# Optimization experiments

Hardware: AMD Instinct MI355X
Metric: run time of the kernel (lower is better)

The kernel has to match this reference:

```python
import jax, jax.numpy as jnp
import numpy as np

B, L, D = 8, 2048, 64


def setup_inputs() -> dict:
    key = jax.random.key(0)
    kq, kk, kv = jax.random.split(key, 3)
    query = jax.random.normal(kq, (B, L, D), dtype=jnp.float32)
    key_t = jax.random.normal(kk, (B, L, D), dtype=jnp.float32)
    value = jax.random.normal(kv, (B, L, D), dtype=jnp.float32)
    return {"query": query, "key": key_t, "value": value}


def reference(query, key, value):
    d = query.shape[-1]
    # e = Q K^T / sqrt(d_k)   -> [B, Lq, Lk]
    scale = 1.0 / np.sqrt(float(d)).astype(np.float32)
    e = jnp.einsum("bqd,bkd->bqk", query, key) * scale
    # stable softmax over keys (matches exp(e - max)/sum in source)
    attention = jax.nn.softmax(e, axis=-1)
    # v = A V   -> [B, Lq, Dv]
    return jnp.einsum("bqk,bkd->bqd", attention, value)
```

## Files before the change

kernel.cpp:

```cpp
#include <hip/hip_runtime.h>


#define B_ 8
#define L_ 2048
#define D_ 64
#define NT 256
#define TK 32

typedef _Float16 half8_t __attribute__((ext_vector_type(8)));
typedef _Float16 half2v __attribute__((ext_vector_type(2)));
typedef int int4v __attribute__((ext_vector_type(4)));
typedef float f32x4 __attribute__((ext_vector_type(4)));

#define SCALE_LOG2E 0.1803368801111244f

__global__ __launch_bounds__(NT) void prepass(
    const float* __restrict__ K, const float* __restrict__ V,
    _Float16* __restrict__ K16, _Float16* __restrict__ VT16)
{
    const int blk = blockIdx.x;
    const int t = threadIdx.x;
    if (blk < 512) {
        const int i = blk * NT + t;
        const float4* s4 = (const float4*)K;
        const float4 a = s4[2 * i], b = s4[2 * i + 1];
        half8_t w;
        w[0] = (_Float16)a.x; w[1] = (_Float16)a.y;
        w[2] = (_Float16)a.z; w[3] = (_Float16)a.w;
        w[4] = (_Float16)b.x; w[5] = (_Float16)b.y;
        w[6] = (_Float16)b.z; w[7] = (_Float16)b.w;
        ((half8_t*)K16)[i] = w;
    } else {
        __shared__ __align__(16) _Float16 Lt[64 * 72];
        const int vblk = blk - 512;
        const int bb = vblk >> 5;
        const int kt = vblk & 31;
        const int r  = t >> 2;
        const int ch = t & 3;
        const float* vrow = V + ((size_t)bb * L_ + kt * 64 + r) * D_ + ch * 16;
        #pragma unroll
        for (int i = 0; i < 4; ++i) {
            const float4 f = ((const float4*)vrow)[i];
            const int d0 = ch * 16 + i * 4;
            Lt[(d0 + 0) * 72 + r] = (_Float16)f.x;
            Lt[(d0 + 1) * 72 + r] = (_Float16)f.y;
            Lt[(d0 + 2) * 72 + r] = (_Float16)f.z;
            Lt[(d0 + 3) * 72 + r] = (_Float16)f.w;
        }
        __syncthreads();
        const int d  = t >> 2;
        const int c2 = t & 3;
        const half8_t w0 = *(const half8_t*)&Lt[d * 72 + c2 * 16];
        const half8_t w1 = *(const half8_t*)&Lt[d * 72 + c2 * 16 + 8];
        _Float16* orow = VT16 + ((size_t)bb * D_ + d) * L_ + kt * 64 + c2 * 16;
        *(half8_t*)orow = w0;
        *(half8_t*)(orow + 8) = w1;
    }
}


#define LOADT(KB, BK, BV)                                                       \
    {                                                                           \
        _Pragma("unroll") for (int s = 0; s < 2; ++s)                           \
        _Pragma("unroll") for (int c = 0; c < 2; ++c)                           \
            BK[s][c] = *(const half8_t*)&Kb[(size_t)((KB) + s * 16 + l15) * D_ + c * 32 + quad * 8]; \
        _Pragma("unroll") for (int d = 0; d < 4; ++d)                           \
            BV[d] = *(const half8_t*)&Vb[(size_t)(d * 16 + l15) * L_ + (KB) + quad * 8]; \
    }

#define PROC(BK, BV)                                                            \
    {                                                                           \
        f32x4 sc[2][2];                                                         \
        _Pragma("unroll") for (int ks = 0; ks < 2; ++ks)                        \
        _Pragma("unroll") for (int qs = 0; qs < 2; ++qs) {                      \
            f32x4 acc = (f32x4){0.f, 0.f, 0.f, 0.f};                            \
            acc = __builtin_amdgcn_mfma_f32_16x16x32_f16(BK[ks][0], bq[qs][0], acc, 0, 0, 0); \
            acc = __builtin_amdgcn_mfma_f32_16x16x32_f16(BK[ks][1], bq[qs][1], acc, 0, 0, 0); \
            sc[ks][qs] = acc;                                                   \
        }                                                                       \
        int pk[2][2][2];                                                        \
        _Pragma("unroll") for (int ks = 0; ks < 2; ++ks)                        \
        _Pragma("unroll") for (int qs = 0; qs < 2; ++qs) {                      \
            const float p0 = __builtin_exp2f(sc[ks][qs][0]);                    \
            const float p1 = __builtin_exp2f(sc[ks][qs][1]);                    \
            const float p2 = __builtin_exp2f(sc[ks][qs][2]);                    \
            const float p3 = __builtin_exp2f(sc[ks][qs][3]);                    \
            lacc[qs] += (p0 + p1) + (p2 + p3);                                  \
            half2v h01; h01[0] = (_Float16)p0; h01[1] = (_Float16)p1;           \
            half2v h23; h23[0] = (_Float16)p2; h23[1] = (_Float16)p3;           \
            pk[ks][qs][0] = __builtin_bit_cast(int, h01);                       \
            pk[ks][qs][1] = __builtin_bit_cast(int, h23);                       \
        }                                                                       \
        _Pragma("unroll") for (int qs = 0; qs < 2; ++qs) {                      \
            const int srcA = ((quad & 1) << 5) + l15;                           \
            const int srcB = srcA + 16;                                         \
            const int a0 = __shfl(pk[0][qs][0], srcA, 64);                      \
            const int b0 = __shfl(pk[1][qs][0], srcA, 64);                      \
            const int a1 = __shfl(pk[0][qs][1], srcA, 64);                      \
            const int b1 = __shfl(pk[1][qs][1], srcA, 64);                      \
            const int a2 = __shfl(pk[0][qs][0], srcB, 64);                      \
            const int b2 = __shfl(pk[1][qs][0], srcB, 64);                      \
            const int a3 = __shfl(pk[0][qs][1], srcB, 64);                      \
            const int b3 = __shfl(pk[1][qs][1], srcB, 64);                      \
            const bool hi = quad >= 2;                                          \
            int4v dw;                                                           \
            dw[0] = hi ? b0 : a0; dw[1] = hi ? b1 : a1;                         \
            dw[2] = hi ? b2 : a2; dw[3] = hi ? b3 : a3;                         \
            const half8_t ap = __builtin_bit_cast(half8_t, dw);                 \
            _Pragma("unroll") for (int d = 0; d < 4; ++d)                       \
                ofr[qs][d] = __builtin_amdgcn_mfma_f32_16x16x32_f16(ap, BV[d], ofr[qs][d], 0, 0, 0); \
        }                                                                       \
    }

__global__ __launch_bounds__(NT) void attn_bp(
    const float* __restrict__ Q,
    const _Float16* __restrict__ K16,
    const _Float16* __restrict__ VT16,
    float* __restrict__ O)
{
    __shared__ float Ored[256 * 33];
    __shared__ float Lred[128];

    const int t    = threadIdx.x;
    const int wave = t >> 6;
    const int lane = t & 63;
    const int quad = lane >> 4;
    const int l15  = lane & 15;

    const int b   = blockIdx.x & 7;
    const int qbi = blockIdx.x >> 3;
    const int qb  = qbi * 32;
    const int key0 = wave * (TK * 16);

    const _Float16* Kb = K16 + (size_t)b * L_ * D_;
    const _Float16* Vb = VT16 + (size_t)b * D_ * L_;

    half8_t bq[2][2];
    #pragma unroll
    for (int qs = 0; qs < 2; ++qs) {
        const float* qp = Q + ((size_t)b * L_ + qb + qs * 16 + l15) * D_ + quad * 8;
        #pragma unroll
        for (int c = 0; c < 2; ++c) {
            const float4 f0 = *(const float4*)(qp + c * 32);
            const float4 f1 = *(const float4*)(qp + c * 32 + 4);
            bq[qs][c][0] = (_Float16)(f0.x * SCALE_LOG2E);
            bq[qs][c][1] = (_Float16)(f0.y * SCALE_LOG2E);
            bq[qs][c][2] = (_Float16)(f0.z * SCALE_LOG2E);
            bq[qs][c][3] = (_Float16)(f0.w * SCALE_LOG2E);
            bq[qs][c][4] = (_Float16)(f1.x * SCALE_LOG2E);
            bq[qs][c][5] = (_Float16)(f1.y * SCALE_LOG2E);
            bq[qs][c][6] = (_Float16)(f1.z * SCALE_LOG2E);
            bq[qs][c][7] = (_Float16)(f1.w * SCALE_LOG2E);
        }
    }

    f32x4 ofr[2][4];
    #pragma unroll
    for (int qs = 0; qs < 2; ++qs)
        #pragma unroll
        for (int d = 0; d < 4; ++d)
            ofr[qs][d] = (f32x4){0.f, 0.f, 0.f, 0.f};
    float lacc[2] = {0.f, 0.f};

    half8_t bkA[2][2], bvA[4], bkB[2][2], bvB[4];
    LOADT(key0, bkA, bvA);
    for (int it = 0; it < 8; ++it) {
        const int kb = key0 + it * 64;
        LOADT(kb + 32, bkB, bvB);
        PROC(bkA, bvA);
        LOADT(kb + 64, bkA, bvA);
        PROC(bkB, bvB);
    }

    #pragma unroll
    for (int qs = 0; qs < 2; ++qs) {
        float v = lacc[qs];
        v += __shfl_xor(v, 16, 64);
        v += __shfl_xor(v, 32, 64);
        lacc[qs] = v;
    }
    if (quad == 0) {
        Lred[wave * 32 + l15] = lacc[0];
        Lred[wave * 32 + 16 + l15] = lacc[1];
    }

    #pragma unroll
    for (int qs = 0; qs < 2; ++qs)
        #pragma unroll
        for (int d = 0; d < 4; ++d)
            #pragma unroll
            for (int r = 0; r < 4; ++r)
                Ored[(wave * 64 + lane) * 33 + qs * 16 + d * 4 + r] = ofr[qs][d][r];
    __syncthreads();

    #pragma unroll
    for (int qs = 0; qs < 2; ++qs)
        #pragma unroll
        for (int r = 0; r < 4; ++r) {
            float osum = 0.f;
            #pragma unroll
            for (int w2 = 0; w2 < 4; ++w2)
                osum += Ored[(w2 * 64 + lane) * 33 + qs * 16 + wave * 4 + r];
            const int row = qs * 16 + quad * 4 + r;
            const float lt = Lred[row] + Lred[32 + row] + Lred[64 + row] + Lred[96 + row];
            O[((size_t)b * L_ + qb + row) * D_ + wave * 16 + l15] = osum / lt;
        }
}

#define KS 72
__global__ __launch_bounds__(NT) void attn_mfma_f16(
    const float* __restrict__ Q, const float* __restrict__ K,
    const float* __restrict__ V, float* __restrict__ O)
{
    __shared__ __align__(16) _Float16 Kt[64 * KS];
    __shared__ __align__(16) _Float16 Vt[D_ * KS];
    __shared__ __align__(16) _Float16 Pt[4][16 * KS];

    const int t = threadIdx.x;
    const int wave = t >> 6, lane = t & 63, quad = lane >> 4, l15 = lane & 15;
    const int bpb = L_ / 64;
    const int b = blockIdx.x / bpb;
    const int qb = (blockIdx.x % bpb) * 64 + wave * 16;
    const size_t boff = (size_t)b * L_ * D_;

    half8_t aq[2];
    {
        const float* qp = Q + boff + (size_t)(qb + l15) * D_ + quad * 8;
        #pragma unroll
        for (int c = 0; c < 2; ++c) {
            const float4* p4 = (const float4*)(qp + c * 32);
            const float4 f0 = p4[0], f1 = p4[1];
            aq[c][0] = (_Float16)f0.x; aq[c][1] = (_Float16)f0.y;
            aq[c][2] = (_Float16)f0.z; aq[c][3] = (_Float16)f0.w;
            aq[c][4] = (_Float16)f1.x; aq[c][5] = (_Float16)f1.y;
            aq[c][6] = (_Float16)f1.z; aq[c][7] = (_Float16)f1.w;
        }
    }
    f32x4 ofr[4];
    #pragma unroll
    for (int d = 0; d < 4; ++d) ofr[d] = (f32x4){0.f, 0.f, 0.f, 0.f};
    float lacc[4] = {0.f, 0.f, 0.f, 0.f};
    const int skey = t & 63, sdg = t >> 6;
    _Float16* Pw = &Pt[wave][0];

    for (int kt = 0; kt < L_ / 64; ++kt) {
        __syncthreads();
        {
            const float4* kg4 = (const float4*)(K + boff + (size_t)(kt * 64 + skey) * D_ + sdg * 16);
            const float4 f0 = kg4[0], f1 = kg4[1], f2 = kg4[2], f3 = kg4[3];
            half8_t w0, w1;
            w0[0] = (_Float16)f0.x; w0[1] = (_Float16)f0.y;
            w0[2] = (_Float16)f0.z; w0[3] = (_Float16)f0.w;
            w0[4] = (_Float16)f1.x; w0[5] = (_Float16)f1.y;
            w0[6] = (_Float16)f1.z; w0[7] = (_Float16)f1.w;
            w1[0] = (_Float16)f2.x; w1[1] = (_Float16)f2.y;
            w1[2] = (_Float16)f2.z; w1[3] = (_Float16)f2.w;
            w1[4] = (_Float16)f3.x; w1[5] = (_Float16)f3.y;
            w1[6] = (_Float16)f3.z; w1[7] = (_Float16)f3.w;
            *(half8_t*)&Kt[skey * KS + sdg * 16] = w0;
            *(half8_t*)&Kt[skey * KS + sdg * 16 + 8] = w1;
        }
        {
            const float4* vg4 = (const float4*)(V + boff + (size_t)(kt * 64 + skey) * D_ + sdg * 16);
            #pragma unroll
            for (int i = 0; i < 4; ++i) {
                const float4 f = vg4[i];
                const int d0 = sdg * 16 + i * 4;
                Vt[(d0 + 0) * KS + skey] = (_Float16)f.x;
                Vt[(d0 + 1) * KS + skey] = (_Float16)f.y;
                Vt[(d0 + 2) * KS + skey] = (_Float16)f.z;
                Vt[(d0 + 3) * KS + skey] = (_Float16)f.w;
            }
        }
        __syncthreads();
        #pragma unroll
        for (int s = 0; s < 4; ++s) {
            const half8_t bk0 = *(const half8_t*)&Kt[(s * 16 + l15) * KS + quad * 8];
            const half8_t bk1 = *(const half8_t*)&Kt[(s * 16 + l15) * KS + 32 + quad * 8];
            f32x4 sc = (f32x4){0.f, 0.f, 0.f, 0.f};
            sc = __builtin_amdgcn_mfma_f32_16x16x32_f16(aq[0], bk0, sc, 0, 0, 0);
            sc = __builtin_amdgcn_mfma_f32_16x16x32_f16(aq[1], bk1, sc, 0, 0, 0);
            #pragma unroll
            for (int r = 0; r < 4; ++r) {
                const float p = __expf(sc[r] * 0.125f);
                lacc[r] += p;
                Pw[(quad * 4 + r) * KS + s * 16 + l15] = (_Float16)p;
            }
        }
        __syncthreads();
        #pragma unroll
        for (int c = 0; c < 2; ++c) {
            const half8_t ap = *(const half8_t*)&Pw[l15 * KS + c * 32 + quad * 8];
            #pragma unroll
            for (int d = 0; d < 4; ++d) {
                const half8_t bv = *(const half8_t*)&Vt[(d * 16 + l15) * KS + c * 32 + quad * 8];
                ofr[d] = __builtin_amdgcn_mfma_f32_16x16x32_f16(ap, bv, ofr[d], 0, 0, 0);
            }
        }
    }
    #pragma unroll
    for (int r = 0; r < 4; ++r) {
        float v = lacc[r];
        v += __shfl_xor(v, 1, 64);
        v += __shfl_xor(v, 2, 64);
        v += __shfl_xor(v, 4, 64);
        v += __shfl_xor(v, 8, 64);
        lacc[r] = v;
    }
    #pragma unroll
    for (int r = 0; r < 4; ++r) {
        const float inv = 1.0f / lacc[r];
        float* orow = O + boff + (size_t)(qb + quad * 4 + r) * D_ + l15;
        #pragma unroll
        for (int d = 0; d < 4; ++d) orow[d * 16] = ofr[d][r] * inv;
    }
}

extern "C" void kernel_launch(void* const* d_in, const int* in_sizes, int n_in,
                              void* d_out, int out_size, void* d_ws, size_t ws_size,
                              hipStream_t stream) {
    const float* Q = (const float*)d_in[0];
    const float* K = (const float*)d_in[1];
    const float* V = (const float*)d_in[2];
    float* O = (float*)d_out;

    if (ws_size >= (size_t)8 * 1024 * 1024) {
        _Float16* K16  = (_Float16*)d_ws;
        _Float16* VT16 = K16 + (size_t)B_ * L_ * D_;
        prepass<<<768, NT, 0, stream>>>(K, V, K16, VT16);
        attn_bp<<<512, NT, 0, stream>>>(Q, K16, VT16, O);
    } else {
        attn_mfma_f16<<<256, NT, 0, stream>>>(Q, K, V, O);
    }
}
```

Baseline: 99.76 us.

## Process 64 queries per block and use 16x16x16 MFMA to drop P shuffles

```diff
diff --git a/kernel.cpp b/kernel.cpp
--- a/kernel.cpp
+++ b/kernel.cpp
@@ -8,8 +8,7 @@
 #define TK 32
 
 typedef _Float16 half8_t __attribute__((ext_vector_type(8)));
-typedef _Float16 half2v __attribute__((ext_vector_type(2)));
-typedef int int4v __attribute__((ext_vector_type(4)));
+typedef _Float16 half4_t __attribute__((ext_vector_type(4)));
 typedef float f32x4 __attribute__((ext_vector_type(4)));
 
 #define SCALE_LOG2E 0.1803368801111244f
@@ -59,67 +58,54 @@
 }
 
 
-#define LOADT(KB, BK, BV)                                                       \
+#define LOADK(KB, BK)                                                           \
     {                                                                           \
         _Pragma("unroll") for (int s = 0; s < 2; ++s)                           \
         _Pragma("unroll") for (int c = 0; c < 2; ++c)                           \
             BK[s][c] = *(const half8_t*)&Kb[(size_t)((KB) + s * 16 + l15) * D_ + c * 32 + quad * 8]; \
+    }
+
+#define PROC(KB, BK)                                                            \
+    {                                                                           \
+        half4_t av[4][2];                                                       \
         _Pragma("unroll") for (int d = 0; d < 4; ++d)                           \
-            BV[d] = *(const half8_t*)&Vb[(size_t)(d * 16 + l15) * L_ + (KB) + quad * 8]; \
-    }
-
-#define PROC(BK, BV)                                                            \
-    {                                                                           \
-        f32x4 sc[2][2];                                                         \
         _Pragma("unroll") for (int ks = 0; ks < 2; ++ks)                        \
-        _Pragma("unroll") for (int qs = 0; qs < 2; ++qs) {                      \
+            av[d][ks] = *(const half4_t*)&Vb[(size_t)(d * 16 + l15) * L_ + (KB) + ks * 16 + quad * 4]; \
+        f32x4 sc[2][4];                                                         \
+        _Pragma("unroll") for (int ks = 0; ks < 2; ++ks)                        \
+        _Pragma("unroll") for (int qs = 0; qs < 4; ++qs) {                      \
             f32x4 acc = (f32x4){0.f, 0.f, 0.f, 0.f};                            \
             acc = __builtin_amdgcn_mfma_f32_16x16x32_f16(BK[ks][0], bq[qs][0], acc, 0, 0, 0); \
             acc = __builtin_amdgcn_mfma_f32_16x16x32_f16(BK[ks][1], bq[qs][1], acc, 0, 0, 0); \
             sc[ks][qs] = acc;                                                   \
         }                                                                       \
-        int pk[2][2][2];                                                        \
+        half4_t pb[2][4];                                                       \
         _Pragma("unroll") for (int ks = 0; ks < 2; ++ks)                        \
-        _Pragma("unroll") for (int qs = 0; qs < 2; ++qs) {                      \
+        _Pragma("unroll") for (int qs = 0; qs < 4; ++qs) {                      \
             const float p0 = __builtin_exp2f(sc[ks][qs][0]);                    \
             const float p1 = __builtin_exp2f(sc[ks][qs][1]);                    \
             const float p2 = __builtin_exp2f(sc[ks][qs][2]);                    \
             const float p3 = __builtin_exp2f(sc[ks][qs][3]);                    \
             lacc[qs] += (p0 + p1) + (p2 + p3);                                  \
-            half2v h01; h01[0] = (_Float16)p0; h01[1] = (_Float16)p1;           \
-            half2v h23; h23[0] = (_Float16)p2; h23[1] = (_Float16)p3;           \
-            pk[ks][qs][0] = __builtin_bit_cast(int, h01);                       \
-            pk[ks][qs][1] = __builtin_bit_cast(int, h23);                       \
+            half4_t pv;                                                         \
+            pv[0] = (_Float16)p0; pv[1] = (_Float16)p1;                         \
+            pv[2] = (_Float16)p2; pv[3] = (_Float16)p3;                         \
+            pb[ks][qs] = pv;                                                    \
         }                                                                       \
-        _Pragma("unroll") for (int qs = 0; qs < 2; ++qs) {                      \
-            const int srcA = ((quad & 1) << 5) + l15;                           \
-            const int srcB = srcA + 16;                                         \
-            const int a0 = __shfl(pk[0][qs][0], srcA, 64);                      \
-            const int b0 = __shfl(pk[1][qs][0], srcA, 64);                      \
-            const int a1 = __shfl(pk[0][qs][1], srcA, 64);                      \
-            const int b1 = __shfl(pk[1][qs][1], srcA, 64);                      \
-            const int a2 = __shfl(pk[0][qs][0], srcB, 64);                      \
-            const int b2 = __shfl(pk[1][qs][0], srcB, 64);                      \
-            const int a3 = __shfl(pk[0][qs][1], srcB, 64);                      \
-            const int b3 = __shfl(pk[1][qs][1], srcB, 64);                      \
-            const bool hi = quad >= 2;                                          \
-            int4v dw;                                                           \
-            dw[0] = hi ? b0 : a0; dw[1] = hi ? b1 : a1;                         \
-            dw[2] = hi ? b2 : a2; dw[3] = hi ? b3 : a3;                         \
-            const half8_t ap = __builtin_bit_cast(half8_t, dw);                 \
-            _Pragma("unroll") for (int d = 0; d < 4; ++d)                       \
-                ofr[qs][d] = __builtin_amdgcn_mfma_f32_16x16x32_f16(ap, BV[d], ofr[qs][d], 0, 0, 0); \
-        }                                                                       \
-    }
-
-__global__ __launch_bounds__(NT) void attn_bp(
+        _Pragma("unroll") for (int qs = 0; qs < 4; ++qs)                        \
+        _Pragma("unroll") for (int d = 0; d < 4; ++d)                           \
+        _Pragma("unroll") for (int ks = 0; ks < 2; ++ks)                        \
+            ofr[qs][d] = __builtin_amdgcn_mfma_f32_16x16x16f16(av[d][ks], pb[ks][qs], ofr[qs][d], 0, 0, 0); \
+    }
+
+__global__ __launch_bounds__(NT) void attn_qs4(
     const float* __restrict__ Q,
     const _Float16* __restrict__ K16,
     const _Float16* __restrict__ VT16,
     float* __restrict__ O)
 {
     __shared__ float Ored[256 * 33];
-    __shared__ float Lred[128];
+    __shared__ float Lred[256];
 
     const int t    = threadIdx.x;
     const int wave = t >> 6;
@@ -129,15 +115,15 @@
 
     const int b   = blockIdx.x & 7;
     const int qbi = blockIdx.x >> 3;
-    const int qb  = qbi * 32;
+    const int qb  = qbi * 64;
     const int key0 = wave * (TK * 16);
 
     const _Float16* Kb = K16 + (size_t)b * L_ * D_;
     const _Float16* Vb = VT16 + (size_t)b * D_ * L_;
 
-    half8_t bq[2][2];
-    #pragma unroll
-    for (int qs = 0; qs < 2; ++qs) {
+    half8_t bq[4][2];
+    #pragma unroll
+    for (int qs = 0; qs < 4; ++qs) {
         const float* qp = Q + ((size_t)b * L_ + qb + qs * 16 + l15) * D_ + quad * 8;
         #pragma unroll
         for (int c = 0; c < 2; ++c) {
@@ -154,57 +140,69 @@
         }
     }
 
-    f32x4 ofr[2][4];
-    #pragma unroll
-    for (int qs = 0; qs < 2; ++qs)
+    f32x4 ofr[4][4];
+    #pragma unroll
+    for (int qs = 0; qs < 4; ++qs)
         #pragma unroll
         for (int d = 0; d < 4; ++d)
             ofr[qs][d] = (f32x4){0.f, 0.f, 0.f, 0.f};
-    float lacc[2] = {0.f, 0.f};
-
-    half8_t bkA[2][2], bvA[4], bkB[2][2], bvB[4];
-    LOADT(key0, bkA, bvA);
+    float lacc[4] = {0.f, 0.f, 0.f, 0.f};
+
+    half8_t bkA[2][2], bkB[2][2];
+    LOADK(key0, bkA);
     for (int it = 0; it < 8; ++it) {
         const int kb = key0 + it * 64;
-        LOADT(kb + 32, bkB, bvB);
-        PROC(bkA, bvA);
-        LOADT(kb + 64, bkA, bvA);
-        PROC(bkB, bvB);
-    }
-
-    #pragma unroll
-    for (int qs = 0; qs < 2; ++qs) {
+        LOADK(kb + 32, bkB);
+        PROC(kb, bkA);
+        LOADK(kb + 64, bkA);
+        PROC(kb + 32, bkB);
+    }
+
+    #pragma unroll
+    for (int qs = 0; qs < 4; ++qs) {
         float v = lacc[qs];
         v += __shfl_xor(v, 16, 64);
         v += __shfl_xor(v, 32, 64);
         lacc[qs] = v;
     }
     if (quad == 0) {
-        Lred[wave * 32 + l15] = lacc[0];
-        Lred[wave * 32 + 16 + l15] = lacc[1];
-    }
-
-    #pragma unroll
-    for (int qs = 0; qs < 2; ++qs)
-        #pragma unroll
-        for (int d = 0; d < 4; ++d)
-            #pragma unroll
-            for (int r = 0; r < 4; ++r)
-                Ored[(wave * 64 + lane) * 33 + qs * 16 + d * 4 + r] = ofr[qs][d][r];
-    __syncthreads();
-
-    #pragma unroll
-    for (int qs = 0; qs < 2; ++qs)
-        #pragma unroll
-        for (int r = 0; r < 4; ++r) {
-            float osum = 0.f;
-            #pragma unroll
-            for (int w2 = 0; w2 < 4; ++w2)
-                osum += Ored[(w2 * 64 + lane) * 33 + qs * 16 + wave * 4 + r];
-            const int row = qs * 16 + quad * 4 + r;
-            const float lt = Lred[row] + Lred[32 + row] + Lred[64 + row] + Lred[96 + row];
-            O[((size_t)b * L_ + qb + row) * D_ + wave * 16 + l15] = osum / lt;
-        }
+        #pragma unroll
+        for (int qs = 0; qs < 4; ++qs)
+            Lred[wave * 64 + qs * 16 + l15] = lacc[qs];
+    }
+
+    #pragma unroll
+    for (int pass = 0; pass < 2; ++pass) {
+        __syncthreads();
+        #pragma unroll
+        for (int qh = 0; qh < 2; ++qh) {
+            const int qs = pass * 2 + qh;
+            #pragma unroll
+            for (int d = 0; d < 4; ++d)
+                #pragma unroll
+                for (int r = 0; r < 4; ++r)
+                    Ored[(wave * 64 + lane) * 33 + qh * 16 + d * 4 + r] = ofr[qs][d][r];
+        }
+        __syncthreads();
+        #pragma unroll
+        for (int qh = 0; qh < 2; ++qh) {
+            const int qs = pass * 2 + qh;
+            const float lt = Lred[qs * 16 + l15] + Lred[64 + qs * 16 + l15]
+                           + Lred[128 + qs * 16 + l15] + Lred[192 + qs * 16 + l15];
+            const float inv = 1.0f / lt;
+            f32x4 osum = (f32x4){0.f, 0.f, 0.f, 0.f};
+            #pragma unroll
+            for (int w2 = 0; w2 < 4; ++w2) {
+                const float* src = &Ored[(w2 * 64 + lane) * 33 + qh * 16 + wave * 4];
+                osum[0] += src[0]; osum[1] += src[1];
+                osum[2] += src[2]; osum[3] += src[3];
+            }
+            float4 outv;
+            outv.x = osum[0] * inv; outv.y = osum[1] * inv;
+            outv.z = osum[2] * inv; outv.w = osum[3] * inv;
+            *(float4*)&O[((size_t)b * L_ + qb + qs * 16 + l15) * D_ + wave * 16 + quad * 4] = outv;
+        }
+    }
 }
 
 #define KS 72
@@ -328,7 +326,7 @@
         _Float16* K16  = (_Float16*)d_ws;
         _Float16* VT16 = K16 + (size_t)B_ * L_ * D_;
         prepass<<<768, NT, 0, stream>>>(K, V, K16, VT16);
-        attn_bp<<<512, NT, 0, stream>>>(Q, K16, VT16, O);
+        attn_qs4<<<256, NT, 0, stream>>>(Q, K16, VT16, O);
     } else {
         attn_mfma_f16<<<256, NT, 0, stream>>>(Q, K, V, O);
     }
```

Measured after the change: 92.36 us. 1.08x faster.
